# Kernel optimization log

Hardware: AMD Instinct MI355X
Metric: run time of the kernel (lower is better)

The kernel has to match this reference:

```python
import jax, jax.numpy as jnp
import numpy as np

N_HEAD = 16


def setup_inputs() -> dict:
    B, T, C, H = 64, 128, 2048, N_HEAD
    hd = C // H
    key = jax.random.key(0)
    ks = jax.random.split(key, 5)
    x = jax.random.normal(ks[0], (B, T, C), dtype=jnp.float32)
    wq = jax.random.normal(ks[1], (C, C), dtype=jnp.float32) * 0.02
    wk = jax.random.normal(ks[2], (C, C), dtype=jnp.float32) * 0.02
    wv = jax.random.normal(ks[3], (C, C), dtype=jnp.float32) * 0.02
    wo = jax.random.normal(ks[4], (C, C), dtype=jnp.float32) * 0.02
    # RoPE frequencies: freqs_cis = exp(i * pos * theta_j), theta_j = 10000^(-2j/hd)
    pos = jnp.arange(T, dtype=jnp.float32)
    inv_freq = 1.0 / (10000.0 ** (jnp.arange(0, hd, 2, dtype=jnp.float32) / hd))  # [hd/2]
    ang = pos[:, None] * inv_freq[None, :]  # [T, hd/2]
    return {
        "x": x,
        "freqs_cos": jnp.cos(ang),
        "freqs_sin": jnp.sin(ang),
        "wq": wq, "wk": wk, "wv": wv, "wo": wo,
    }


def _apply_rope(t, cos, sin):
    # t: [B,T,H,hd]; complex multiply on interleaved (even, odd) pairs
    B, T, H, hd = t.shape
    tr = t.reshape(B, T, H, hd // 2, 2)
    te, to = tr[..., 0], tr[..., 1]
    c = cos[None, :, None, :]  # [1,T,1,hd/2]
    s = sin[None, :, None, :]
    oe = te * c - to * s
    oo = te * s + to * c
    return jnp.stack([oe, oo], axis=-1).reshape(B, T, H, hd)


def reference(x, freqs_cos, freqs_sin, wq, wk, wv, wo):
    B, T, C = x.shape
    H = N_HEAD
    hd = C // H
    q = (x @ wq.T).reshape(B, T, H, hd)
    k = (x @ wk.T).reshape(B, T, H, hd)
    v = (x @ wv.T).reshape(B, T, H, hd)
    q = _apply_rope(q, freqs_cos, freqs_sin)
    k = _apply_rope(k, freqs_cos, freqs_sin)
    # scores: [B,H,T,S]
    scores = jnp.einsum("bthd,bshd->bhts", q, k) / (hd ** 0.5)
    causal = jnp.tril(jnp.ones((T, T), dtype=bool))
    scores = jnp.where(causal[None, None], scores, jnp.float32(-jnp.inf))
    probs = jax.nn.softmax(scores, axis=-1)  # dropout is identity in eval
    out = jnp.einsum("bhts,bshd->bthd", probs, v).reshape(B, T, C)
    return out @ wo.T
```

## Files before the change

kernel.cpp:

```cpp
#include <hip/hip_runtime.h>
#include <cstdint>


typedef unsigned short ushort;
typedef __bf16 bf16x8 __attribute__((ext_vector_type(8)));
typedef float floatx4 __attribute__((ext_vector_type(4)));

__device__ __forceinline__ ushort f2bf(float f) {
  union { float f; uint32_t u; } v; v.f = f;
  uint32_t r = v.u + 0x7FFFu + ((v.u >> 16) & 1u);
  return (ushort)(r >> 16);
}
__device__ __forceinline__ float bf2f(ushort h) {
  union { uint32_t u; float f; } v; v.u = ((uint32_t)h) << 16;
  return v.f;
}

__device__ __forceinline__ void load_lds16(const void* g, void* l) {
  __builtin_amdgcn_global_load_lds(
      (__attribute__((address_space(1))) void*)(uintptr_t)g,
      (__attribute__((address_space(3))) void*)(uint32_t)(uintptr_t)l,
      16, 0, 0);
}

__device__ __forceinline__ void store_out(ushort* C, size_t i, float v) { C[i] = f2bf(v); }
__device__ __forceinline__ void store_out(float* C, size_t i, float v) { C[i] = v; }

__device__ __forceinline__ void phase_mid() {
  __builtin_amdgcn_s_barrier();
  asm volatile("s_waitcnt lgkmcnt(0)" ::: "memory");
  __builtin_amdgcn_sched_barrier(0);
}
__device__ __forceinline__ void phase_end() {
  __builtin_amdgcn_s_barrier();
  __builtin_amdgcn_sched_barrier(0);
}

template <typename OutT>
__device__ __forceinline__ void gemm256_body(const ushort* __restrict__ A,
                                             const ushort* __restrict__ B,
                                             OutT* __restrict__ C,
                                             int M, int N, int K) {
  (void)M;
  __shared__ __align__(16) ushort As[2][256 * 64];
  __shared__ __align__(16) ushort Bs[2][256 * 64];
  const int tid = threadIdx.x;
  const int wave = tid >> 6, lane = tid & 63;
  const int quad = lane >> 4, colv = lane & 15;
  const int wm = wave & 1, wn = wave >> 1;
  const int m0 = blockIdx.x * 256, n0 = blockIdx.y * 256;

  const int a_base = (wm * 128 + colv) * 64;
  const int b_base = (wn * 64 + colv) * 64;
  const int kg0 = ((quad) ^ (colv & 7)) << 3;
  const int kg1 = ((quad | 4) ^ (colv & 7)) << 3;

  const int srow = tid >> 3;
  const int scol = ((tid & 7) ^ (srow & 7)) << 3;
  const ushort* Ag = A + (size_t)(m0 + srow) * K + scol;
  const ushort* Bg = B + (size_t)(n0 + srow) * K + scol;
  const int ldsw = wave * 512;

  floatx4 acc[8][4] = {};
  bf16x8 af[4][2], bfr[4][2];

#define STAGE(Gb, T, half, kt)                                             \
  {                                                                        \
    const ushort* g_ = (Gb) + (size_t)((half) * 128) * K + (kt) * 64;      \
    load_lds16(g_, &(T)[(half) * 8192 + ldsw]);                            \
    load_lds16(g_ + (size_t)64 * K, &(T)[(half) * 8192 + 4096 + ldsw]);    \
  }

#define READ_B_ALL(bi)                                                     \
  _Pragma("unroll") for (int nf = 0; nf < 4; ++nf) {                       \
    bfr[nf][0] = *(const bf16x8*)&Bs[bi][b_base + nf * 1024 + kg0];        \
    bfr[nf][1] = *(const bf16x8*)&Bs[bi][b_base + nf * 1024 + kg1];        \
  }

#define READ_A(bi, off)                                                    \
  _Pragma("unroll") for (int mf = 0; mf < 4; ++mf) {                       \
    af[mf][0] = *(const bf16x8*)&As[bi][a_base + (off) + mf * 1024 + kg0]; \
    af[mf][1] = *(const bf16x8*)&As[bi][a_base + (off) + mf * 1024 + kg1]; \
  }

#define MFMA16(ks, mo)                                                     \
  __builtin_amdgcn_s_setprio(1);                                           \
  _Pragma("unroll") for (int mf = 0; mf < 4; ++mf)                         \
  _Pragma("unroll") for (int nf = 0; nf < 4; ++nf)                         \
    acc[(mo) + mf][nf] = __builtin_amdgcn_mfma_f32_16x16x32_bf16(          \
        af[mf][(ks)], bfr[nf][(ks)], acc[(mo) + mf][nf], 0, 0, 0);         \
  __builtin_amdgcn_s_setprio(0);

  STAGE(Bg, Bs[0], 0, 0)
  STAGE(Bg, Bs[0], 1, 0)
  STAGE(Ag, As[0], 0, 0)
  STAGE(Ag, As[0], 1, 0)
  STAGE(Bg, Bs[1], 0, 1)
  STAGE(Bg, Bs[1], 1, 1)
  STAGE(Ag, As[1], 0, 1)
  asm volatile("s_waitcnt vmcnt(6)" ::: "memory");
  __builtin_amdgcn_s_barrier();
  __builtin_amdgcn_sched_barrier(0);

  const int NT = K >> 6;
#pragma unroll 1
  for (int it = 0; it < (NT >> 1); ++it) {
    const int s0 = (2 * it + 2 < NT) ? 2 * it + 2 : NT - 1;
    const int s1 = (2 * it + 3 < NT) ? 2 * it + 3 : NT - 1;

    READ_B_ALL(0)
    READ_A(0, 0)
    STAGE(Ag, As[1], 1, 2 * it + 1)
    phase_mid();
    MFMA16(0, 0)
    phase_end();
    STAGE(Bg, Bs[0], 0, s0)
    phase_mid();
    MFMA16(1, 0)
    phase_end();
    READ_A(0, 4096)
    STAGE(Bg, Bs[0], 1, s0)
    phase_mid();
    MFMA16(0, 4)
    phase_end();
    STAGE(Ag, As[0], 0, s0)
    asm volatile("s_waitcnt vmcnt(6)" ::: "memory");
    phase_mid();
    MFMA16(1, 4)
    phase_end();
    READ_B_ALL(1)
    READ_A(1, 0)
    STAGE(Ag, As[0], 1, s0)
    phase_mid();
    MFMA16(0, 0)
    phase_end();
    STAGE(Bg, Bs[1], 0, s1)
    phase_mid();
    MFMA16(1, 0)
    phase_end();
    READ_A(1, 4096)
    STAGE(Bg, Bs[1], 1, s1)
    phase_mid();
    MFMA16(0, 4)
    phase_end();
    STAGE(Ag, As[1], 0, s1)
    asm volatile("s_waitcnt vmcnt(6)" ::: "memory");
    phase_mid();
    MFMA16(1, 4)
    phase_end();
  }
  asm volatile("s_waitcnt vmcnt(0)" ::: "memory");

#pragma unroll
  for (int mf = 0; mf < 8; ++mf)
#pragma unroll
    for (int nf = 0; nf < 4; ++nf)
#pragma unroll
      for (int r = 0; r < 4; ++r) {
        int m = m0 + wm * 128 + mf * 16 + quad * 4 + r;
        int n = n0 + wn * 64 + nf * 16 + colv;
        store_out(C, (size_t)m * N + n, acc[mf][nf][r]);
      }
#undef STAGE
#undef READ_B_ALL
#undef READ_A
#undef MFMA16
}

__global__ __launch_bounds__(512) void gemm_qkv(
    const ushort* __restrict__ A, const ushort* __restrict__ Wq,
    const ushort* __restrict__ Wk, const ushort* __restrict__ Wv,
    ushort* __restrict__ Q, ushort* __restrict__ Kb, ushort* __restrict__ V) {
  const ushort* B = (blockIdx.z == 0) ? Wq : (blockIdx.z == 1) ? Wk : Wv;
  ushort* C = (blockIdx.z == 0) ? Q : (blockIdx.z == 1) ? Kb : V;
  gemm256_body<ushort>(A, B, C, 8192, 2048, 2048);
}

__global__ __launch_bounds__(512) void gemm_out_k(
    const ushort* __restrict__ A, const ushort* __restrict__ B,
    float* __restrict__ C) {
  gemm256_body<float>(A, B, C, 8192, 2048, 2048);
}

#define NX4  4194304u
#define NW4  1048576u
__global__ __launch_bounds__(256) void cvt_all(
    const float* __restrict__ x, const float* __restrict__ wq,
    const float* __restrict__ wk, const float* __restrict__ wv,
    const float* __restrict__ wo,
    ushort* __restrict__ xb, ushort* __restrict__ wqb,
    ushort* __restrict__ wkb, ushort* __restrict__ wvb,
    ushort* __restrict__ wob) {
  const uint32_t i0 = blockIdx.x * 256u + threadIdx.x;
#pragma unroll
  for (uint32_t u = 0; u < 16u; ++u) {
    uint32_t i = i0 + u * 524288u;
    const float* src;
    ushort* dst;
    uint32_t off;
    if (i < NX4) {
      src = x; dst = xb; off = i;
    } else {
      uint32_t i2 = i - NX4;
      uint32_t r = i2 >> 20;
      off = i2 & (NW4 - 1u);
      src = (r == 0) ? wq : (r == 1) ? wk : (r == 2) ? wv : wo;
      dst = (r == 0) ? wqb : (r == 1) ? wkb : (r == 2) ? wvb : wob;
    }
    float4 v = ((const float4*)src)[off];
    ushort4 o;
    o.x = f2bf(v.x); o.y = f2bf(v.y); o.z = f2bf(v.z); o.w = f2bf(v.w);
    ((ushort4*)dst)[off] = o;
  }
}

__global__ __launch_bounds__(256, 2) void attn_kernel(
    const ushort* __restrict__ Q, const ushort* __restrict__ K,
    const ushort* __restrict__ V, const float* __restrict__ Cf,
    const float* __restrict__ Sf, ushort* __restrict__ O) {
  __shared__ __align__(16) ushort Qs[128 * 136];
  __shared__ __align__(16) ushort KVs[128 * 128];
  const int b = blockIdx.x >> 4, h = blockIdx.x & 15;
  const int tid = threadIdx.x, wave = tid >> 6, lane = tid & 63;
  const int quad = lane >> 4, colv = lane & 15;
  const size_t gbase = (size_t)b * 262144 + (size_t)h * 128;

  uint4 vreg[8];
#pragma unroll
  for (int sgi = 0; sgi < 8; ++sgi) {
    int seg = tid + sgi * 256;
    int t = seg >> 4, g = seg & 15;
    uint4 qv = *(const uint4*)(Q + gbase + (size_t)t * 2048 + g * 8);
    uint4 kv = *(const uint4*)(K + gbase + (size_t)t * 2048 + g * 8);
    vreg[sgi] = *(const uint4*)(V + gbase + (size_t)t * 2048 + g * 8);
    float4 cf = *(const float4*)(Cf + t * 64 + g * 4);
    float4 sf = *(const float4*)(Sf + t * 64 + g * 4);
    uint32_t* qw = (uint32_t*)&qv;
    uint32_t* kw = (uint32_t*)&kv;
#pragma unroll
    for (int j = 0; j < 4; ++j) {
      float c = (&cf.x)[j], s = (&sf.x)[j];
      uint32_t w = qw[j];
      float e = bf2f((ushort)(w & 0xFFFF)), o = bf2f((ushort)(w >> 16));
      qw[j] = (uint32_t)f2bf(e * c - o * s) | ((uint32_t)f2bf(e * s + o * c) << 16);
      w = kw[j];
      e = bf2f((ushort)(w & 0xFFFF)); o = bf2f((ushort)(w >> 16));
      kw[j] = (uint32_t)f2bf(e * c - o * s) | ((uint32_t)f2bf(e * s + o * c) << 16);
    }
    int so = t * 128 + ((g ^ (t & 15)) << 3);
    *(uint4*)&Qs[so] = qv;
    *(uint4*)&KVs[so] = kv;
  }
  __syncthreads();

  floatx4 accs[2][8] = {};
#pragma unroll
  for (int kc = 0; kc < 4; ++kc) {
    bf16x8 af[2], bfr[8];
#pragma unroll
    for (int i = 0; i < 2; ++i) {
      int r = wave * 32 + i * 16 + colv;
      af[i] = *(const bf16x8*)&Qs[r * 128 + ((((kc << 2) | quad) ^ (r & 15)) << 3)];
    }
#pragma unroll
    for (int j = 0; j < 8; ++j) {
      int r = j * 16 + colv;
      bfr[j] = *(const bf16x8*)&KVs[r * 128 + ((((kc << 2) | quad) ^ (r & 15)) << 3)];
    }
    __builtin_amdgcn_s_setprio(1);
#pragma unroll
    for (int i = 0; i < 2; ++i)
#pragma unroll
      for (int j = 0; j < 8; ++j)
        accs[i][j] = __builtin_amdgcn_mfma_f32_16x16x32_bf16(af[i], bfr[j], accs[i][j], 0, 0, 0);
    __builtin_amdgcn_s_setprio(0);
  }
  __syncthreads();

#pragma unroll
  for (int sgi = 0; sgi < 8; ++sgi) {
    int seg = tid + sgi * 256;
    int t = seg >> 4;
    int dg = (seg & 15) << 3;
    const ushort* vp = (const ushort*)&vreg[sgi];
#pragma unroll
    for (int jj = 0; jj < 8; ++jj) {
      int d = dg + jj;
      KVs[d * 128 + ((((t >> 3) ^ (d & 15)) << 3) | (t & 7))] = vp[jj];
    }
  }

  const float scale = 0.08838834764831845f;
#pragma unroll
  for (int i = 0; i < 2; ++i)
#pragma unroll
    for (int r = 0; r < 4; ++r) {
      int t = wave * 32 + i * 16 + quad * 4 + r;
      float mx = -1e30f;
#pragma unroll
      for (int j = 0; j < 8; ++j) {
        int s = j * 16 + colv;
        float v = accs[i][j][r] * scale;
        v = (s <= t) ? v : -1e30f;
        accs[i][j][r] = v;
        mx = fmaxf(mx, v);
      }
#pragma unroll
      for (int off = 1; off < 16; off <<= 1) mx = fmaxf(mx, __shfl_xor(mx, off, 64));
      float l = 0.f;
#pragma unroll
      for (int j = 0; j < 8; ++j) {
        float p = __expf(accs[i][j][r] - mx);
        accs[i][j][r] = p;
        l += p;
      }
#pragma unroll
      for (int off = 1; off < 16; off <<= 1) l += __shfl_xor(l, off, 64);
      float inv = 1.0f / l;
#pragma unroll
      for (int j = 0; j < 8; ++j) {
        int s = j * 16 + colv;
        Qs[t * 128 + ((((s >> 3) ^ (t & 15)) << 3) | (s & 7))] = f2bf(accs[i][j][r] * inv);
      }
    }
  __syncthreads();

  floatx4 acco[2][8] = {};
#pragma unroll
  for (int kc = 0; kc < 4; ++kc) {
    bf16x8 af[2], bfr[8];
#pragma unroll
    for (int i = 0; i < 2; ++i) {
      int r = wave * 32 + i * 16 + colv;
      af[i] = *(const bf16x8*)&Qs[r * 128 + ((((kc << 2) | quad) ^ (r & 15)) << 3)];
    }
#pragma unroll
    for (int j = 0; j < 8; ++j) {
      int r = j * 16 + colv;
      bfr[j] = *(const bf16x8*)&KVs[r * 128 + ((((kc << 2) | quad) ^ (r & 15)) << 3)];
    }
    __builtin_amdgcn_s_setprio(1);
#pragma unroll
    for (int i = 0; i < 2; ++i)
#pragma unroll
      for (int j = 0; j < 8; ++j)
        acco[i][j] = __builtin_amdgcn_mfma_f32_16x16x32_bf16(af[i], bfr[j], acco[i][j], 0, 0, 0);
    __builtin_amdgcn_s_setprio(0);
  }
  __syncthreads();

#pragma unroll
  for (int i = 0; i < 2; ++i)
#pragma unroll
    for (int j = 0; j < 8; ++j)
#pragma unroll
      for (int r = 0; r < 4; ++r) {
        int t = wave * 32 + i * 16 + quad * 4 + r;
        int d = j * 16 + colv;
        Qs[t * 136 + d] = f2bf(acco[i][j][r]);
      }
#pragma unroll
  for (int g = 0; g < 8; ++g) {
    int row = wave * 32 + g * 4 + quad;
    uint4 ov = *(const uint4*)&Qs[row * 136 + colv * 8];
    *(uint4*)(O + gbase + (size_t)row * 2048 + colv * 8) = ov;
  }
}

extern "C" void kernel_launch(void* const* d_in, const int* in_sizes, int n_in,
                              void* d_out, int out_size, void* d_ws, size_t ws_size,
                              hipStream_t stream) {
  const float* x    = (const float*)d_in[0];
  const float* fcos = (const float*)d_in[1];
  const float* fsin = (const float*)d_in[2];
  const float* wq   = (const float*)d_in[3];
  const float* wk   = (const float*)d_in[4];
  const float* wv   = (const float*)d_in[5];
  const float* wo   = (const float*)d_in[6];
  float* out = (float*)d_out;

  const size_t CC = 2048ull * 2048ull;
  const size_t MC = 8192ull * 2048ull;
  ushort* wob = (ushort*)d_ws;
  ushort* xb  = wob + CC;
  ushort* wqb = xb + MC;
  ushort* wkb = wqb + CC;
  ushort* wvb = wkb + CC;
  ushort* Qb  = wvb + CC;
  ushort* Kb  = Qb + MC;
  ushort* Vb  = Kb + MC;

  cvt_all<<<dim3(2048), 256, 0, stream>>>(x, wq, wk, wv, wo, xb, wqb, wkb, wvb, wob);

  gemm_qkv<<<dim3(32, 8, 3), 512, 0, stream>>>(xb, wqb, wkb, wvb, Qb, Kb, Vb);
  attn_kernel<<<dim3(1024), 256, 0, stream>>>(Qb, Kb, Vb, fcos, fsin, xb);
  gemm_out_k<<<dim3(32, 8), 512, 0, stream>>>(xb, wob, out);
}
```

Before: 448.4 us.

## Switch GEMM inner loop to 32x32x16 MFMA and split QKV launch

```diff
diff --git a/kernel.cpp b/kernel.cpp
--- a/kernel.cpp
+++ b/kernel.cpp
@@ -5,6 +5,7 @@
 typedef unsigned short ushort;
 typedef __bf16 bf16x8 __attribute__((ext_vector_type(8)));
 typedef float floatx4 __attribute__((ext_vector_type(4)));
+typedef float floatx16 __attribute__((ext_vector_type(16)));
 
 __device__ __forceinline__ ushort f2bf(float f) {
   union { float f; uint32_t u; } v; v.f = f;
@@ -46,14 +47,23 @@
   __shared__ __align__(16) ushort Bs[2][256 * 64];
   const int tid = threadIdx.x;
   const int wave = tid >> 6, lane = tid & 63;
-  const int quad = lane >> 4, colv = lane & 15;
+  const int lane31 = lane & 31, lane5 = lane >> 5, l7 = lane & 7;
   const int wm = wave & 1, wn = wave >> 1;
   const int m0 = blockIdx.x * 256, n0 = blockIdx.y * 256;
 
-  const int a_base = (wm * 128 + colv) * 64;
-  const int b_base = (wn * 64 + colv) * 64;
-  const int kg0 = ((quad) ^ (colv & 7)) << 3;
-  const int kg1 = ((quad | 4) ^ (colv & 7)) << 3;
+  int a_off[4][4], b_off[2][4];
+#pragma unroll
+  for (int mb = 0; mb < 4; ++mb)
+#pragma unroll
+    for (int ks = 0; ks < 4; ++ks)
+      a_off[mb][ks] = (wm * 128 + mb * 32 + lane31) * 64 +
+                      (((2 * ks + lane5) ^ l7) << 3);
+#pragma unroll
+  for (int nb = 0; nb < 2; ++nb)
+#pragma unroll
+    for (int ks = 0; ks < 4; ++ks)
+      b_off[nb][ks] = (wn * 64 + nb * 32 + lane31) * 64 +
+                      (((2 * ks + lane5) ^ l7) << 3);
 
   const int srow = tid >> 3;
   const int scol = ((tid & 7) ^ (srow & 7)) << 3;
@@ -61,8 +71,8 @@
   const ushort* Bg = B + (size_t)(n0 + srow) * K + scol;
   const int ldsw = wave * 512;
 
-  floatx4 acc[8][4] = {};
-  bf16x8 af[4][2], bfr[4][2];
+  floatx16 acc[4][2] = {};
+  bf16x8 af[2][4], bfr[2][4];
 
 #define STAGE(Gb, T, half, kt)                                             \
   {                                                                        \
@@ -72,23 +82,23 @@
   }
 
 #define READ_B_ALL(bi)                                                     \
-  _Pragma("unroll") for (int nf = 0; nf < 4; ++nf) {                       \
-    bfr[nf][0] = *(const bf16x8*)&Bs[bi][b_base + nf * 1024 + kg0];        \
-    bfr[nf][1] = *(const bf16x8*)&Bs[bi][b_base + nf * 1024 + kg1];        \
-  }
-
-#define READ_A(bi, off)                                                    \
-  _Pragma("unroll") for (int mf = 0; mf < 4; ++mf) {                       \
-    af[mf][0] = *(const bf16x8*)&As[bi][a_base + (off) + mf * 1024 + kg0]; \
-    af[mf][1] = *(const bf16x8*)&As[bi][a_base + (off) + mf * 1024 + kg1]; \
-  }
-
-#define MFMA16(ks, mo)                                                     \
+  _Pragma("unroll") for (int nb = 0; nb < 2; ++nb)                         \
+  _Pragma("unroll") for (int ks = 0; ks < 4; ++ks)                         \
+    bfr[nb][ks] = *(const bf16x8*)&Bs[bi][b_off[nb][ks]];
+
+#define READ_A_HALF(bi, half)                                              \
+  _Pragma("unroll") for (int j = 0; j < 2; ++j)                            \
+  _Pragma("unroll") for (int ks = 0; ks < 4; ++ks)                         \
+    af[j][ks] = *(const bf16x8*)&As[bi][a_off[(half) * 2 + j][ks]];
+
+#define MFMA8(kp, mh)                                                      \
   __builtin_amdgcn_s_setprio(1);                                           \
-  _Pragma("unroll") for (int mf = 0; mf < 4; ++mf)                         \
-  _Pragma("unroll") for (int nf = 0; nf < 4; ++nf)                         \
-    acc[(mo) + mf][nf] = __builtin_amdgcn_mfma_f32_16x16x32_bf16(          \
-        af[mf][(ks)], bfr[nf][(ks)], acc[(mo) + mf][nf], 0, 0, 0);         \
+  _Pragma("unroll") for (int j = 0; j < 2; ++j)                            \
+  _Pragma("unroll") for (int nb = 0; nb < 2; ++nb)                         \
+  _Pragma("unroll") for (int k2 = 0; k2 < 2; ++k2)                         \
+    acc[(mh) * 2 + j][nb] = __builtin_amdgcn_mfma_f32_32x32x16_bf16(       \
+        af[j][(kp) * 2 + k2], bfr[nb][(kp) * 2 + k2],                      \
+        acc[(mh) * 2 + j][nb], 0, 0, 0);                                   \
   __builtin_amdgcn_s_setprio(0);
 
   STAGE(Bg, Bs[0], 0, 0)
@@ -109,71 +119,68 @@
     const int s1 = (2 * it + 3 < NT) ? 2 * it + 3 : NT - 1;
 
     READ_B_ALL(0)
-    READ_A(0, 0)
+    READ_A_HALF(0, 0)
     STAGE(Ag, As[1], 1, 2 * it + 1)
     phase_mid();
-    MFMA16(0, 0)
+    MFMA8(0, 0)
     phase_end();
     STAGE(Bg, Bs[0], 0, s0)
     phase_mid();
-    MFMA16(1, 0)
-    phase_end();
-    READ_A(0, 4096)
+    MFMA8(1, 0)
+    phase_end();
+    READ_A_HALF(0, 1)
     STAGE(Bg, Bs[0], 1, s0)
     phase_mid();
-    MFMA16(0, 4)
+    MFMA8(0, 1)
     phase_end();
     STAGE(Ag, As[0], 0, s0)
     asm volatile("s_waitcnt vmcnt(6)" ::: "memory");
     phase_mid();
-    MFMA16(1, 4)
+    MFMA8(1, 1)
     phase_end();
     READ_B_ALL(1)
-    READ_A(1, 0)
+    READ_A_HALF(1, 0)
     STAGE(Ag, As[0], 1, s0)
     phase_mid();
-    MFMA16(0, 0)
+    MFMA8(0, 0)
     phase_end();
     STAGE(Bg, Bs[1], 0, s1)
     phase_mid();
-    MFMA16(1, 0)
-    phase_end();
-    READ_A(1, 4096)
+    MFMA8(1, 0)
+    phase_end();
+    READ_A_HALF(1, 1)
     STAGE(Bg, Bs[1], 1, s1)
     phase_mid();
-    MFMA16(0, 4)
+    MFMA8(0, 1)
     phase_end();
     STAGE(Ag, As[1], 0, s1)
     asm volatile("s_waitcnt vmcnt(6)" ::: "memory");
     phase_mid();
-    MFMA16(1, 4)
+    MFMA8(1, 1)
     phase_end();
   }
   asm volatile("s_waitcnt vmcnt(0)" ::: "memory");
 
 #pragma unroll
-  for (int mf = 0; mf < 8; ++mf)
-#pragma unroll
-    for (int nf = 0; nf < 4; ++nf)
-#pragma unroll
-      for (int r = 0; r < 4; ++r) {
-        int m = m0 + wm * 128 + mf * 16 + quad * 4 + r;
-        int n = n0 + wn * 64 + nf * 16 + colv;
-        store_out(C, (size_t)m * N + n, acc[mf][nf][r]);
+  for (int mb = 0; mb < 4; ++mb)
+#pragma unroll
+    for (int nb = 0; nb < 2; ++nb)
+#pragma unroll
+      for (int reg = 0; reg < 16; ++reg) {
+        int m = m0 + wm * 128 + mb * 32 + (reg & 3) + 8 * (reg >> 2) + 4 * lane5;
+        int n = n0 + wn * 64 + nb * 32 + lane31;
+        store_out(C, (size_t)m * N + n, acc[mb][nb][reg]);
       }
 #undef STAGE
 #undef READ_B_ALL
-#undef READ_A
-#undef MFMA16
-}
-
-__global__ __launch_bounds__(512) void gemm_qkv(
-    const ushort* __restrict__ A, const ushort* __restrict__ Wq,
-    const ushort* __restrict__ Wk, const ushort* __restrict__ Wv,
-    ushort* __restrict__ Q, ushort* __restrict__ Kb, ushort* __restrict__ V) {
-  const ushort* B = (blockIdx.z == 0) ? Wq : (blockIdx.z == 1) ? Wk : Wv;
-  ushort* C = (blockIdx.z == 0) ? Q : (blockIdx.z == 1) ? Kb : V;
-  gemm256_body<ushort>(A, B, C, 8192, 2048, 2048);
+#undef READ_A_HALF
+#undef MFMA8
+}
+
+__global__ __launch_bounds__(512) void gemm_bt16(
+    const ushort* __restrict__ A, const ushort* __restrict__ W,
+    ushort* __restrict__ C) {
+  gemm256_body<ushort>(A, W, C, 8192, 2048, 2048);
 }
 
 __global__ __launch_bounds__(512) void gemm_out_k(
@@ -392,7 +399,9 @@
 
   cvt_all<<<dim3(2048), 256, 0, stream>>>(x, wq, wk, wv, wo, xb, wqb, wkb, wvb, wob);
 
-  gemm_qkv<<<dim3(32, 8, 3), 512, 0, stream>>>(xb, wqb, wkb, wvb, Qb, Kb, Vb);
+  gemm_bt16<<<dim3(32, 8), 512, 0, stream>>>(xb, wqb, Qb);
+  gemm_bt16<<<dim3(32, 8), 512, 0, stream>>>(xb, wkb, Kb);
+  gemm_bt16<<<dim3(32, 8), 512, 0, stream>>>(xb, wvb, Vb);
   attn_kernel<<<dim3(1024), 256, 0, stream>>>(Qb, Kb, Vb, fcos, fsin, xb);
   gemm_out_k<<<dim3(32, 8), 512, 0, stream>>>(xb, wob, out);
 }
```

Result: slower. 481.3 us (+7.3%).
